# Optimization experiments

Measured on AMD Instinct MI355X. Metric: run time of the kernel, lower is better.

## Reference

```python
import jax, jax.numpy as jnp
import numpy as np

N = 100_000          # nodes
E = 1_600_000        # edges (avg degree 16)
NODE_SCA, NODE_VEC = 4, 3
EDGE_SCA, EDGE_VEC = 6, 3
OUT_SCA, OUT_VEC = 16, 16
CUTOFF = 10.0
EPS = 1e-6
SLOPE_VN = 0.2       # VNLeakyReLU negative slope (SurfGen default)
SLOPE_SCA = 0.01     # nn.LeakyReLU default


def setup_inputs() -> dict:
    key = jax.random.key(0)
    ks = jax.random.split(key, 22)
    rn = lambda k, s: jax.random.normal(k, s, dtype=jnp.float32)
    return {
        # forward args
        'node_sca': rn(ks[0], (N, NODE_SCA)),
        'node_vec': rn(ks[1], (N, NODE_VEC, 3)),
        'edge_sca': rn(ks[2], (E, EDGE_SCA)),
        'edge_vec': rn(ks[3], (E, EDGE_VEC, 3)),
        'gds_dist': jax.random.uniform(ks[4], (E,), dtype=jnp.float32) * 12.0,
        'edge_index': jax.random.randint(ks[5], (2, E), 0, N),
        # message projections (Linear weights stored [in,out])
        'W_nss': rn(ks[6], (NODE_SCA, OUT_SCA)) * 0.3, 'b_nss': rn(ks[7], (OUT_SCA,)) * 0.1,
        'W_ess': rn(ks[8], (EDGE_SCA, OUT_SCA)) * 0.3, 'b_ess': rn(ks[9], (OUT_SCA,)) * 0.1,
        'W_nsv': rn(ks[10], (NODE_SCA, OUT_SCA)) * 0.3, 'b_nsv': rn(ks[11], (OUT_SCA,)) * 0.1,
        'W_esv': rn(ks[12], (EDGE_SCA, OUT_SCA)) * 0.3, 'b_esv': rn(ks[13], (OUT_SCA,)) * 0.1,
        'W_nvv': rn(ks[14], (NODE_VEC, OUT_VEC)) * 0.3,   # VNLinear (no bias)
        'W_evv': rn(ks[15], (EDGE_VEC, OUT_VEC)) * 0.3,
        # GVPerceptronVN(16,16,16,16): GVLinear (dim_hid = 16) + VN LeakyReLU
        'W_lv':  rn(ks[16], (OUT_VEC, OUT_VEC)) * 0.25,   # lin_vector   (no bias)
        'W_lv2': rn(ks[17], (OUT_VEC, OUT_VEC)) * 0.25,   # lin_vector2  (no bias)
        'W_ls':  rn(ks[18], (OUT_VEC + OUT_SCA, OUT_SCA)) * 0.25,  # lin_scalar (no bias)
        'W_gate': rn(ks[19], (OUT_SCA, OUT_VEC)) * 0.25, 'b_gate': rn(ks[20], (OUT_VEC,)) * 0.1,
        'W_dir': rn(ks[21], (OUT_VEC, OUT_VEC)) * 0.25,   # VNLeakyReLU direction (no bias)
    }


def vn_linear(x, W):
    # x: [n, c_in, 3], W: [c_in, c_out] -> [n, c_out, 3]
    return jnp.einsum('nci,co->noi', x, W)


def reference(node_sca, node_vec, edge_sca, edge_vec, gds_dist, edge_index,
              W_nss, b_nss, W_ess, b_ess, W_nsv, b_nsv, W_esv, b_esv,
              W_nvv, W_evv, W_lv, W_lv2, W_ls, W_gate, b_gate, W_dir):
    src = edge_index[0]
    num_nodes = node_sca.shape[0]

    # cosine cutoff coefficient
    coeff = 0.5 * (jnp.cos(gds_dist * (jnp.pi / CUTOFF)) + 1.0)
    coeff = coeff * (gds_dist <= CUTOFF) * (gds_dist >= 0.0)  # [E]

    # scalar message: gather node proj, mix with edge proj, cutoff-weight
    node_ss = node_sca @ W_nss + b_nss                          # [N,16]
    edge_ss = edge_sca @ W_ess + b_ess                          # [E,16]
    msg_sca = node_ss[src] * edge_ss * coeff[:, None]           # [E,16]

    # vector message
    node_vv = vn_linear(node_vec, W_nvv)                        # [N,16,3]
    edge_vv = vn_linear(edge_vec, W_evv)                        # [E,16,3]
    node_sv = node_sca @ W_nsv + b_nsv                          # [N,16]
    edge_sv = edge_sca @ W_esv + b_esv                          # [E,16]
    msg_vec = (node_vv[src] * edge_sv[:, :, None]
               + node_sv[src][:, :, None] * edge_vv) * coeff[:, None, None]  # [E,16,3]

    # scatter_sum into source nodes (matches original's edge_index[0])
    aggr_sca = jax.ops.segment_sum(msg_sca, src, num_segments=num_nodes)  # [N,16]
    aggr_vec = jax.ops.segment_sum(msg_vec, src, num_segments=num_nodes)  # [N,16,3]

    # --- GVPerceptronVN: GVLinear ---
    v_inter = vn_linear(aggr_vec, W_lv)                          # [N,16,3]
    v_norm = jnp.sqrt(jnp.sum(v_inter * v_inter, axis=-1))       # [N,16]
    out_sca = jnp.concatenate([v_norm, aggr_sca], axis=-1) @ W_ls  # [N,16]
    out_vec = vn_linear(v_inter, W_lv2)                          # [N,16,3]
    gate = jax.nn.sigmoid(out_sca @ W_gate + b_gate)[:, :, None]
    out_vec = gate * out_vec

    # --- VNLeakyReLU on vectors ---
    d = vn_linear(out_vec, W_dir)                                # [N,16,3]
    dot = jnp.sum(out_vec * d, axis=-1, keepdims=True)
    mask = (dot >= 0).astype(out_vec.dtype)
    d_norm_sq = jnp.sum(d * d, axis=-1, keepdims=True)
    out_vec = SLOPE_VN * out_vec + (1.0 - SLOPE_VN) * (
        mask * out_vec + (1.0 - mask) * (out_vec - (dot / (d_norm_sq + EPS)) * d))

    # LeakyReLU on scalars
    out_sca = jnp.where(out_sca >= 0, out_sca, SLOPE_SCA * out_sca)
    return out_sca, out_vec
```

## Files before the change

### kernel.cpp

```cpp
#include <hip/hip_runtime.h>
#include <math.h>

#define CUTOFF_F 10.0f
#define PI_OVER_CUTOFF 0.31415926535897931f
#define KID 32

__global__ __launch_bounds__(256) void fill_ids(
    const float* __restrict__ gds,
    const int* __restrict__ eidx,
    const float* __restrict__ edge_sca,
    const float* __restrict__ edge_vec,
    int* __restrict__ count,
    int* __restrict__ bucket,
    float* __restrict__ aggr,
    int E)
{
    int e = blockIdx.x * blockDim.x + threadIdx.x;
    if (e >= E) return;

    float d = gds[e];
    if (d > CUTOFF_F || d < 0.0f) return;

    int src = eidx[e];
    int slot = atomicAdd(&count[src], 1);
    if (slot < KID) {
        bucket[(size_t)src * KID + slot] = e;
    } else {
        float c = 0.5f * (__cosf(d * PI_OVER_CUTOFF) + 1.0f);
        const float* es = edge_sca + (size_t)e * 6;
        const float* ev = edge_vec + (size_t)e * 9;
        float* base = aggr + (size_t)src * 16;
#pragma unroll
        for (int i = 0; i < 6; ++i) atomicAdd(base + i, c * es[i]);
        atomicAdd(base + 6, c);
#pragma unroll
        for (int i = 0; i < 9; ++i) atomicAdd(base + 7 + i, c * ev[i]);
    }
}

__global__ __launch_bounds__(256) void edge_aggregate(
    const float* __restrict__ edge_sca, const float* __restrict__ edge_vec,
    const float* __restrict__ gds, const int* __restrict__ eidx,
    float* __restrict__ aggr, int E)
{
    int e = blockIdx.x * blockDim.x + threadIdx.x;
    if (e >= E) return;
    int src = eidx[e];
    float d = gds[e];
    float coeff = 0.0f;
    if (d >= 0.0f && d <= CUTOFF_F)
        coeff = 0.5f * (__cosf(d * PI_OVER_CUTOFF) + 1.0f);
    float* base = aggr + (size_t)src * 16;
    const float* es = edge_sca + (size_t)e * 6;
    const float* ev = edge_vec + (size_t)e * 9;
#pragma unroll
    for (int c = 0; c < 6; ++c) atomicAdd(base + c, coeff * es[c]);
    atomicAdd(base + 6, coeff);
#pragma unroll
    for (int k = 0; k < 9; ++k) atomicAdd(base + 7 + k, coeff * ev[k]);
}

__global__ __launch_bounds__(256) void node_fused(
    const float* __restrict__ node_sca,
    const float* __restrict__ node_vec,
    const float* __restrict__ edge_sca,
    const float* __restrict__ edge_vec,
    const float* __restrict__ gds,
    const int* __restrict__ count,
    const int* __restrict__ bucket,
    const float* __restrict__ aggr,
    const float* __restrict__ W_nss, const float* __restrict__ b_nss,
    const float* __restrict__ W_ess, const float* __restrict__ b_ess,
    const float* __restrict__ W_nsv, const float* __restrict__ b_nsv,
    const float* __restrict__ W_esv, const float* __restrict__ b_esv,
    const float* __restrict__ W_nvv, const float* __restrict__ W_evv,
    const float* __restrict__ W_lv,  const float* __restrict__ W_lv2,
    const float* __restrict__ W_ls,
    const float* __restrict__ W_gate, const float* __restrict__ b_gate,
    const float* __restrict__ W_dir,
    float* __restrict__ out,
    int N, int mode)
{
    __shared__ float sW_nss[64],  sb_nss[16];
    __shared__ float sW_ess[96],  sb_ess[16];
    __shared__ float sW_nsv[64],  sb_nsv[16];
    __shared__ float sW_esv[96],  sb_esv[16];
    __shared__ float sW_nvv[48],  sW_evv[48];
    __shared__ float sW_lv[256],  sW_lv2[256];
    __shared__ float sW_ls[512];
    __shared__ float sW_gate[256], sb_gate[16];
    __shared__ float sW_dir[256];

    __shared__ float s_in  [16 * 33];
    __shared__ float s_avec[16 * 49];
    __shared__ float s_cat [16 * 33];
    __shared__ float s_vint[16 * 49];
    __shared__ float s_osca[16 * 17];
    __shared__ float s_ovec[16 * 49];

    __shared__ int   s_eid[KID * 17];
    __shared__ float s_ec [KID * 17];

    const int t = threadIdx.x;
    {
        for (int i = t; i < 64;  i += 256) { sW_nss[i] = W_nss[i]; sW_nsv[i] = W_nsv[i]; }
        for (int i = t; i < 96;  i += 256) { sW_ess[i] = W_ess[i]; sW_esv[i] = W_esv[i]; }
        for (int i = t; i < 48;  i += 256) { sW_nvv[i] = W_nvv[i]; sW_evv[i] = W_evv[i]; }
        for (int i = t; i < 256; i += 256) {
            sW_lv[i]   = W_lv[i];
            sW_lv2[i]  = W_lv2[i];
            sW_gate[i] = W_gate[i];
            sW_dir[i]  = W_dir[i];
        }
        for (int i = t; i < 512; i += 256) sW_ls[i] = W_ls[i];
        if (t < 16) {
            sb_nss[t]  = b_nss[t];
            sb_ess[t]  = b_ess[t];
            sb_nsv[t]  = b_nsv[t];
            sb_esv[t]  = b_esv[t];
            sb_gate[t] = b_gate[t];
        }
    }

    const int slot = t >> 4;
    const int o    = t & 15;
    const int n    = blockIdx.x * 16 + slot;
    const bool valid = (n < N);

    if (valid) {
        if (o < 4) s_in[slot * 33 + o]     = node_sca[(size_t)n * 4 + o];
        if (o < 9) s_in[slot * 33 + 4 + o] = node_vec[(size_t)n * 9 + o];
    }

    if (mode == 4) {
        int cnt = 0;
        if (valid) {
            cnt = count[n];
            if (cnt > KID) cnt = KID;
            const int* bk = bucket + (size_t)n * KID;
            for (int s = o; s < cnt; s += 16) {
                int e = bk[s];
                float d = gds[e];
                s_eid[s * 17 + slot] = e;
                s_ec [s * 17 + slot] = 0.5f * (__cosf(d * PI_OVER_CUTOFF) + 1.0f);
            }
        }
        __syncthreads();
        if (valid) {
            float acc = aggr[(size_t)n * 16 + o];
            const float* fsrc = (o < 6) ? edge_sca : edge_vec;
            const int    st   = (o < 6) ? 6 : 9;
            const int    off  = (o < 6) ? o : (o - 7);
            for (int s = 0; s < cnt; ++s) {
                int   e = s_eid[s * 17 + slot];
                float c = s_ec [s * 17 + slot];
                float f = (o == 6) ? 1.0f : fsrc[(size_t)e * st + off];
                acc += c * f;
            }
            s_in[slot * 33 + 13 + o] = acc;
        }
    } else {
        if (valid) s_in[slot * 33 + 13 + o] = aggr[(size_t)n * 16 + o];
    }
    __syncthreads();

    const float* in = s_in + slot * 33;

    float nss = sb_nss[o], nsv = sb_nsv[o];
#pragma unroll
    for (int c = 0; c < 4; ++c) {
        float x = in[c];
        nss += x * sW_nss[c * 16 + o];
        nsv += x * sW_nsv[c * 16 + o];
    }
    float nvv0 = 0.f, nvv1 = 0.f, nvv2 = 0.f;
#pragma unroll
    for (int c = 0; c < 3; ++c) {
        float w = sW_nvv[c * 16 + o];
        nvv0 += in[4 + c * 3 + 0] * w;
        nvv1 += in[4 + c * 3 + 1] * w;
        nvv2 += in[4 + c * 3 + 2] * w;
    }
    float cc = in[19];
    float es = cc * sb_ess[o], ev = cc * sb_esv[o];
#pragma unroll
    for (int c = 0; c < 6; ++c) {
        float a = in[13 + c];
        es += a * sW_ess[c * 16 + o];
        ev += a * sW_esv[c * 16 + o];
    }
    float EV0 = 0.f, EV1 = 0.f, EV2 = 0.f;
#pragma unroll
    for (int c = 0; c < 3; ++c) {
        float w = sW_evv[c * 16 + o];
        EV0 += in[20 + c * 3 + 0] * w;
        EV1 += in[20 + c * 3 + 1] * w;
        EV2 += in[20 + c * 3 + 2] * w;
    }

    float asca = nss * es;
    float av0 = nvv0 * ev + nsv * EV0;
    float av1 = nvv1 * ev + nsv * EV1;
    float av2 = nvv2 * ev + nsv * EV2;
    s_avec[slot * 49 + o * 3 + 0] = av0;
    s_avec[slot * 49 + o * 3 + 1] = av1;
    s_avec[slot * 49 + o * 3 + 2] = av2;
    s_cat[slot * 33 + 16 + o] = asca;
    __syncthreads();

    float vi0 = 0.f, vi1 = 0.f, vi2 = 0.f;
#pragma unroll
    for (int c = 0; c < 16; ++c) {
        float w = sW_lv[c * 16 + o];
        const float* a = &s_avec[slot * 49 + c * 3];
        vi0 += a[0] * w; vi1 += a[1] * w; vi2 += a[2] * w;
    }
    float vnorm = sqrtf(vi0 * vi0 + vi1 * vi1 + vi2 * vi2);
    s_vint[slot * 49 + o * 3 + 0] = vi0;
    s_vint[slot * 49 + o * 3 + 1] = vi1;
    s_vint[slot * 49 + o * 3 + 2] = vi2;
    s_cat[slot * 33 + o] = vnorm;
    __syncthreads();

    float osca = 0.f;
#pragma unroll
    for (int c = 0; c < 32; ++c)
        osca += s_cat[slot * 33 + c] * sW_ls[c * 16 + o];
    float ov0 = 0.f, ov1 = 0.f, ov2 = 0.f;
#pragma unroll
    for (int c = 0; c < 16; ++c) {
        float w = sW_lv2[c * 16 + o];
        const float* a = &s_vint[slot * 49 + c * 3];
        ov0 += a[0] * w; ov1 += a[1] * w; ov2 += a[2] * w;
    }
    s_osca[slot * 17 + o] = osca;
    __syncthreads();

    float g = sb_gate[o];
#pragma unroll
    for (int c = 0; c < 16; ++c)
        g += s_osca[slot * 17 + c] * sW_gate[c * 16 + o];
    g = 1.0f / (1.0f + __expf(-g));
    ov0 *= g; ov1 *= g; ov2 *= g;
    s_ovec[slot * 49 + o * 3 + 0] = ov0;
    s_ovec[slot * 49 + o * 3 + 1] = ov1;
    s_ovec[slot * 49 + o * 3 + 2] = ov2;
    __syncthreads();

    float dv0 = 0.f, dv1 = 0.f, dv2 = 0.f;
#pragma unroll
    for (int c = 0; c < 16; ++c) {
        float w = sW_dir[c * 16 + o];
        const float* a = &s_ovec[slot * 49 + c * 3];
        dv0 += a[0] * w; dv1 += a[1] * w; dv2 += a[2] * w;
    }
    float dot = ov0 * dv0 + ov1 * dv1 + ov2 * dv2;
    if (dot < 0.0f) {
        float dn = dv0 * dv0 + dv1 * dv1 + dv2 * dv2;
        float f = 0.8f * dot / (dn + 1e-6f);
        ov0 -= f * dv0; ov1 -= f * dv1; ov2 -= f * dv2;
    }

    if (valid) {
        float so = (osca >= 0.0f) ? osca : 0.01f * osca;
        out[(size_t)n * 16 + o] = so;
        size_t vb = (size_t)N * 16 + (size_t)n * 48 + (size_t)o * 3;
        out[vb + 0] = ov0;
        out[vb + 1] = ov1;
        out[vb + 2] = ov2;
    }
}

extern "C" void kernel_launch(void* const* d_in, const int* in_sizes, int n_in,
                              void* d_out, int out_size, void* d_ws, size_t ws_size,
                              hipStream_t stream)
{
    const float* node_sca = (const float*)d_in[0];
    const float* node_vec = (const float*)d_in[1];
    const float* edge_sca = (const float*)d_in[2];
    const float* edge_vec = (const float*)d_in[3];
    const float* gds      = (const float*)d_in[4];
    const int*   eidx     = (const int*)d_in[5];

    const int N = in_sizes[0] / 4;
    const int E = in_sizes[4];

    int*   count4  = (int*)d_ws;
    float* aggr4   = (float*)(count4 + N);
    int*   bucket4 = (int*)(aggr4 + (size_t)N * 16);
    size_t need4   = (size_t)N * 4 + (size_t)N * 64 + (size_t)N * KID * 4;

    float* aggr0  = (float*)d_ws;
    size_t need0  = (size_t)N * 64;

    if (ws_size >= need4) {
        hipMemsetAsync(count4, 0, (size_t)N * 4 + (size_t)N * 64, stream);
        fill_ids<<<(E + 255) / 256, 256, 0, stream>>>(
            gds, eidx, edge_sca, edge_vec, count4, bucket4, aggr4, E);
        node_fused<<<(N + 15) / 16, 256, 0, stream>>>(
            node_sca, node_vec, edge_sca, edge_vec, gds,
            count4, bucket4, aggr4,
            (const float*)d_in[6],  (const float*)d_in[7],
            (const float*)d_in[8],  (const float*)d_in[9],
            (const float*)d_in[10], (const float*)d_in[11],
            (const float*)d_in[12], (const float*)d_in[13],
            (const float*)d_in[14], (const float*)d_in[15],
            (const float*)d_in[16], (const float*)d_in[17],
            (const float*)d_in[18],
            (const float*)d_in[19], (const float*)d_in[20],
            (const float*)d_in[21],
            (float*)d_out, N, 4);
        return;
    }

    (void)need0;
    hipMemsetAsync(aggr0, 0, (size_t)N * 64, stream);
    edge_aggregate<<<(E + 255) / 256, 256, 0, stream>>>(
        edge_sca, edge_vec, gds, eidx, aggr0, E);
    node_fused<<<(N + 15) / 16, 256, 0, stream>>>(
        node_sca, node_vec, edge_sca, edge_vec, gds,
        (const int*)d_ws, (const int*)d_ws, aggr0,
        (const float*)d_in[6],  (const float*)d_in[7],
        (const float*)d_in[8],  (const float*)d_in[9],
        (const float*)d_in[10], (const float*)d_in[11],
        (const float*)d_in[12], (const float*)d_in[13],
        (const float*)d_in[14], (const float*)d_in[15],
        (const float*)d_in[16], (const float*)d_in[17],
        (const float*)d_in[18],
        (const float*)d_in[19], (const float*)d_in[20],
        (const float*)d_in[21],
        (float*)d_out, N, 0);
}
```

Measured before the change: 335.4 us.

## Scatter precomputed per-edge payloads into per-node slots instead of edge ids

Adds a scatter kernel that uses 16 threads per edge. It computes the cutoff-weighted 16-float payload (6 scalars, the coefficient, 9 vector components) and writes it contiguously into a per-node slot buffer, with overflow going to atomics. The node kernel's new mode then sums these contiguous slots directly, replacing the gather by edge id of scattered edge_sca/edge_vec rows and the shared id/coefficient staging (those buffers now alias other shared arrays). The cost is much larger workspace use (N*KIDr*64 bytes) and extra write traffic in exchange for coalesced reads. The path runs only if the workspace allows at least 16 slots per node.

```diff
diff --git a/kernel.cpp b/kernel.cpp
--- a/kernel.cpp
+++ b/kernel.cpp
@@ -4,6 +4,42 @@
 #define CUTOFF_F 10.0f
 #define PI_OVER_CUTOFF 0.31415926535897931f
 #define KID 32
+
+__global__ __launch_bounds__(256) void scatter_f32(
+    const float* __restrict__ gds,
+    const int* __restrict__ eidx,
+    const float* __restrict__ edge_sca,
+    const float* __restrict__ edge_vec,
+    int* __restrict__ count,
+    float* __restrict__ payload,
+    float* __restrict__ aggr,
+    int E, int KIDr)
+{
+    int t = blockIdx.x * blockDim.x + threadIdx.x;
+    int e = t >> 4;
+    int o = t & 15;
+    if (e >= E) return;
+
+    float d = gds[e];
+    if (d > CUTOFF_F || d < 0.0f) return;
+
+    float c = 0.5f * (__cosf(d * PI_OVER_CUTOFF) + 1.0f);
+    float f;
+    if (o < 6)       f = c * edge_sca[(size_t)e * 6 + o];
+    else if (o == 6) f = c;
+    else             f = c * edge_vec[(size_t)e * 9 + (o - 7)];
+
+    int src = eidx[e];
+    int slot = 0;
+    if (o == 0) slot = atomicAdd(&count[src], 1);
+    slot = __shfl(slot, 0, 16);
+
+    if (slot < KIDr) {
+        payload[((size_t)src * KIDr + slot) * 16 + o] = f;
+    } else {
+        atomicAdd(&aggr[(size_t)src * 16 + o], f);
+    }
+}
 
 __global__ __launch_bounds__(256) void fill_ids(
     const float* __restrict__ gds,
@@ -68,6 +104,7 @@
     const float* __restrict__ gds,
     const int* __restrict__ count,
     const int* __restrict__ bucket,
+    const float* __restrict__ payload,
     const float* __restrict__ aggr,
     const float* __restrict__ W_nss, const float* __restrict__ b_nss,
     const float* __restrict__ W_ess, const float* __restrict__ b_ess,
@@ -79,7 +116,7 @@
     const float* __restrict__ W_gate, const float* __restrict__ b_gate,
     const float* __restrict__ W_dir,
     float* __restrict__ out,
-    int N, int mode)
+    int N, int mode, int KIDr)
 {
     __shared__ float sW_nss[64],  sb_nss[16];
     __shared__ float sW_ess[96],  sb_ess[16];
@@ -98,8 +135,8 @@
     __shared__ float s_osca[16 * 17];
     __shared__ float s_ovec[16 * 49];
 
-    __shared__ int   s_eid[KID * 17];
-    __shared__ float s_ec [KID * 17];
+    int*   s_eid = (int*)s_vint;
+    float* s_ec  = s_ovec;
 
     const int t = threadIdx.x;
     {
@@ -132,7 +169,25 @@
         if (o < 9) s_in[slot * 33 + 4 + o] = node_vec[(size_t)n * 9 + o];
     }
 
-    if (mode == 4) {
+    if (mode == 5) {
+        if (valid) {
+            int cnt = count[n];
+            if (cnt > KIDr) cnt = KIDr;
+            const float* p = payload + (size_t)n * KIDr * 16 + o;
+            float a0 = 0.f, a1 = 0.f, a2 = 0.f, a3 = 0.f;
+            int s = 0;
+            for (; s + 3 < cnt; s += 4) {
+                a0 += p[(s + 0) * 16];
+                a1 += p[(s + 1) * 16];
+                a2 += p[(s + 2) * 16];
+                a3 += p[(s + 3) * 16];
+            }
+            for (; s < cnt; ++s)
+                a0 += p[s * 16];
+            a1 += aggr[(size_t)n * 16 + o];
+            s_in[slot * 33 + 13 + o] = (a0 + a1) + (a2 + a3);
+        }
+    } else if (mode == 4) {
         int cnt = 0;
         if (valid) {
             cnt = count[n];
@@ -285,21 +340,26 @@
     const int N = in_sizes[0] / 4;
     const int E = in_sizes[4];
 
-    int*   count4  = (int*)d_ws;
-    float* aggr4   = (float*)(count4 + N);
-    int*   bucket4 = (int*)(aggr4 + (size_t)N * 16);
-    size_t need4   = (size_t)N * 4 + (size_t)N * 64 + (size_t)N * KID * 4;
-
-    float* aggr0  = (float*)d_ws;
-    size_t need0  = (size_t)N * 64;
-
-    if (ws_size >= need4) {
-        hipMemsetAsync(count4, 0, (size_t)N * 4 + (size_t)N * 64, stream);
-        fill_ids<<<(E + 255) / 256, 256, 0, stream>>>(
-            gds, eidx, edge_sca, edge_vec, count4, bucket4, aggr4, E);
+    int*   countp = (int*)d_ws;
+    float* aggrp  = (float*)(countp + N);
+    size_t hdr    = (size_t)N * 4 + (size_t)N * 64;
+
+    float* payload5 = (float*)((char*)d_ws + hdr);
+    int KIDr = 0;
+    if (ws_size > hdr)
+        KIDr = (int)((ws_size - hdr) / ((size_t)N * 64));
+    if (KIDr > 32) KIDr = 32;
+
+    int*   bucket4 = (int*)((char*)d_ws + hdr);
+    size_t need4   = hdr + (size_t)N * KID * 4;
+
+    if (KIDr >= 16) {
+        hipMemsetAsync(countp, 0, hdr, stream);
+        scatter_f32<<<(int)(((size_t)E * 16 + 255) / 256), 256, 0, stream>>>(
+            gds, eidx, edge_sca, edge_vec, countp, payload5, aggrp, E, KIDr);
         node_fused<<<(N + 15) / 16, 256, 0, stream>>>(
             node_sca, node_vec, edge_sca, edge_vec, gds,
-            count4, bucket4, aggr4,
+            countp, bucket4, payload5, aggrp,
             (const float*)d_in[6],  (const float*)d_in[7],
             (const float*)d_in[8],  (const float*)d_in[9],
             (const float*)d_in[10], (const float*)d_in[11],
@@ -309,17 +369,37 @@
             (const float*)d_in[18],
             (const float*)d_in[19], (const float*)d_in[20],
             (const float*)d_in[21],
-            (float*)d_out, N, 4);
+            (float*)d_out, N, 5, KIDr);
         return;
     }
 
-    (void)need0;
+    if (ws_size >= need4) {
+        hipMemsetAsync(countp, 0, hdr, stream);
+        fill_ids<<<(E + 255) / 256, 256, 0, stream>>>(
+            gds, eidx, edge_sca, edge_vec, countp, bucket4, aggrp, E);
+        node_fused<<<(N + 15) / 16, 256, 0, stream>>>(
+            node_sca, node_vec, edge_sca, edge_vec, gds,
+            countp, bucket4, payload5, aggrp,
+            (const float*)d_in[6],  (const float*)d_in[7],
+            (const float*)d_in[8],  (const float*)d_in[9],
+            (const float*)d_in[10], (const float*)d_in[11],
+            (const float*)d_in[12], (const float*)d_in[13],
+            (const float*)d_in[14], (const float*)d_in[15],
+            (const float*)d_in[16], (const float*)d_in[17],
+            (const float*)d_in[18],
+            (const float*)d_in[19], (const float*)d_in[20],
+            (const float*)d_in[21],
+            (float*)d_out, N, 4, 0);
+        return;
+    }
+
+    float* aggr0 = (float*)d_ws;
     hipMemsetAsync(aggr0, 0, (size_t)N * 64, stream);
     edge_aggregate<<<(E + 255) / 256, 256, 0, stream>>>(
         edge_sca, edge_vec, gds, eidx, aggr0, E);
     node_fused<<<(N + 15) / 16, 256, 0, stream>>>(
         node_sca, node_vec, edge_sca, edge_vec, gds,
-        (const int*)d_ws, (const int*)d_ws, aggr0,
+        (const int*)d_ws, (const int*)d_ws, (const float*)d_ws, aggr0,
         (const float*)d_in[6],  (const float*)d_in[7],
         (const float*)d_in[8],  (const float*)d_in[9],
         (const float*)d_in[10], (const float*)d_in[11],
@@ -329,5 +409,5 @@
         (const float*)d_in[18],
         (const float*)d_in[19], (const float*)d_in[20],
         (const float*)d_in[21],
-        (float*)d_out, N, 0);
+        (float*)d_out, N, 0, 0);
 }
```

Measured after the change: 399.2 us. +19.0%, slower.

## Replace per-node edge buckets with per-block coarse buckets and LDS reduction

Applied to the files above, without the earlier changes.

Edges are appended to coarse buckets of 98 nodes each, storing the cutoff-weighted 16-float features contiguously. Each node-block then reduces its bucket into shared memory with LDS atomics and processes its 98 nodes in 7 tiles. This replaces the per-node id buckets, which forced scattered gathers of edge features in the node kernel, with streaming reads of precomputed features. The costs are a larger workspace, heavy contention on one global counter per bucket, and sequential tiles that lengthen each block's work.

```diff
diff --git a/kernel.cpp b/kernel.cpp
--- a/kernel.cpp
+++ b/kernel.cpp
@@ -3,38 +3,55 @@
 
 #define CUTOFF_F 10.0f
 #define PI_OVER_CUTOFF 0.31415926535897931f
-#define KID 32
-
-__global__ __launch_bounds__(256) void fill_ids(
+#define NPB    98
+#define NTILES 7
+
+__global__ __launch_bounds__(256) void bucket_append(
     const float* __restrict__ gds,
     const int* __restrict__ eidx,
     const float* __restrict__ edge_sca,
     const float* __restrict__ edge_vec,
-    int* __restrict__ count,
-    int* __restrict__ bucket,
-    float* __restrict__ aggr,
-    int E)
+    int* __restrict__ bcnt,
+    int* __restrict__ flag,
+    float* __restrict__ aggr_ovf,
+    int* __restrict__ ids,
+    float* __restrict__ feats,
+    int E, int cap)
 {
-    int e = blockIdx.x * blockDim.x + threadIdx.x;
+    int e = blockIdx.x * 256 + threadIdx.x;
     if (e >= E) return;
 
     float d = gds[e];
-    if (d > CUTOFF_F || d < 0.0f) return;
-
+    if (d < 0.0f || d > CUTOFF_F) return;
+
+    float c = 0.5f * (__cosf(d * PI_OVER_CUTOFF) + 1.0f);
     int src = eidx[e];
-    int slot = atomicAdd(&count[src], 1);
-    if (slot < KID) {
-        bucket[(size_t)src * KID + slot] = e;
+    const float* es = edge_sca + (size_t)e * 6;
+    const float* ev = edge_vec + (size_t)e * 9;
+
+    float f[16];
+#pragma unroll
+    for (int i = 0; i < 6; ++i) f[i] = c * es[i];
+    f[6] = c;
+#pragma unroll
+    for (int i = 0; i < 9; ++i) f[7 + i] = c * ev[i];
+
+    int b = src / NPB;
+    int slot = atomicAdd(&bcnt[b * 16], 1);
+
+    if (slot < cap) {
+        size_t r = (size_t)b * cap + slot;
+        ids[r] = src;
+        float4* pr = (float4*)(feats + r * 16);
+        pr[0] = make_float4(f[0],  f[1],  f[2],  f[3]);
+        pr[1] = make_float4(f[4],  f[5],  f[6],  f[7]);
+        pr[2] = make_float4(f[8],  f[9],  f[10], f[11]);
+        pr[3] = make_float4(f[12], f[13], f[14], f[15]);
     } else {
-        float c = 0.5f * (__cosf(d * PI_OVER_CUTOFF) + 1.0f);
-        const float* es = edge_sca + (size_t)e * 6;
-        const float* ev = edge_vec + (size_t)e * 9;
-        float* base = aggr + (size_t)src * 16;
-#pragma unroll
-        for (int i = 0; i < 6; ++i) atomicAdd(base + i, c * es[i]);
-        atomicAdd(base + 6, c);
-#pragma unroll
-        for (int i = 0; i < 9; ++i) atomicAdd(base + 7 + i, c * ev[i]);
+        flag[0] = 1;
+        float* bb = aggr_ovf + (size_t)src * 16;
+#pragma unroll
+        for (int i = 0; i < 16; ++i) atomicAdd(bb + i, f[i]);
     }
 }
 
@@ -60,15 +77,14 @@
     for (int k = 0; k < 9; ++k) atomicAdd(base + 7 + k, coeff * ev[k]);
 }
 
-__global__ __launch_bounds__(256) void node_fused(
+__global__ __launch_bounds__(256) void bucket_reduce_node(
     const float* __restrict__ node_sca,
     const float* __restrict__ node_vec,
-    const float* __restrict__ edge_sca,
-    const float* __restrict__ edge_vec,
-    const float* __restrict__ gds,
-    const int* __restrict__ count,
-    const int* __restrict__ bucket,
-    const float* __restrict__ aggr,
+    const int* __restrict__ bcnt,
+    const int* __restrict__ flag,
+    const float* __restrict__ aggr_ovf,
+    const int* __restrict__ ids,
+    const float* __restrict__ feats,
     const float* __restrict__ W_nss, const float* __restrict__ b_nss,
     const float* __restrict__ W_ess, const float* __restrict__ b_ess,
     const float* __restrict__ W_nsv, const float* __restrict__ b_nsv,
@@ -79,7 +95,7 @@
     const float* __restrict__ W_gate, const float* __restrict__ b_gate,
     const float* __restrict__ W_dir,
     float* __restrict__ out,
-    int N, int mode)
+    int N, int cap, int forceOvf)
 {
     __shared__ float sW_nss[64],  sb_nss[16];
     __shared__ float sW_ess[96],  sb_ess[16];
@@ -91,15 +107,14 @@
     __shared__ float sW_gate[256], sb_gate[16];
     __shared__ float sW_dir[256];
 
+    __shared__ float s_aggr[NPB * 17];
+
     __shared__ float s_in  [16 * 33];
     __shared__ float s_avec[16 * 49];
     __shared__ float s_cat [16 * 33];
     __shared__ float s_vint[16 * 49];
     __shared__ float s_osca[16 * 17];
     __shared__ float s_ovec[16 * 49];
-
-    __shared__ int   s_eid[KID * 17];
-    __shared__ float s_ec [KID * 17];
 
     const int t = threadIdx.x;
     {
@@ -121,153 +136,155 @@
             sb_gate[t] = b_gate[t];
         }
     }
-
-    const int slot = t >> 4;
-    const int o    = t & 15;
-    const int n    = blockIdx.x * 16 + slot;
-    const bool valid = (n < N);
-
-    if (valid) {
-        if (o < 4) s_in[slot * 33 + o]     = node_sca[(size_t)n * 4 + o];
-        if (o < 9) s_in[slot * 33 + 4 + o] = node_vec[(size_t)n * 9 + o];
-    }
-
-    if (mode == 4) {
-        int cnt = 0;
+    for (int i = t; i < NPB * 17; i += 256) s_aggr[i] = 0.0f;
+    __syncthreads();
+
+    const int b     = blockIdx.x;
+    const int node0 = b * NPB;
+    const int g     = t >> 4;
+    const int o     = t & 15;
+
+    if (!forceOvf) {
+        int cnt = bcnt[b * 16];
+        if (cnt > cap) cnt = cap;
+        size_t rb = (size_t)b * cap;
+        for (int r = g; r < cnt; r += 16) {
+            int src = ids[rb + r];
+            float v = feats[(rb + r) * 16 + o];
+            atomicAdd(&s_aggr[(src - node0) * 17 + o], v);
+        }
+    }
+    __syncthreads();
+
+    int useOvf = forceOvf | flag[0];
+    if (useOvf) {
+        for (int idx = t; idx < NPB * 16; idx += 256) {
+            int nn = idx >> 4, oo = idx & 15;
+            int n = node0 + nn;
+            if (n < N) s_aggr[nn * 17 + oo] += aggr_ovf[(size_t)n * 16 + oo];
+        }
+    }
+    __syncthreads();
+
+    for (int tile = 0; tile < NTILES; ++tile) {
+        const int slotn = tile * 16 + g;
+        const int n     = node0 + slotn;
+        const bool valid = (slotn < NPB) && (n < N);
+        const int slot = g;
+
         if (valid) {
-            cnt = count[n];
-            if (cnt > KID) cnt = KID;
-            const int* bk = bucket + (size_t)n * KID;
-            for (int s = o; s < cnt; s += 16) {
-                int e = bk[s];
-                float d = gds[e];
-                s_eid[s * 17 + slot] = e;
-                s_ec [s * 17 + slot] = 0.5f * (__cosf(d * PI_OVER_CUTOFF) + 1.0f);
-            }
-        }
-        __syncthreads();
+            if (o < 4) s_in[slot * 33 + o]     = node_sca[(size_t)n * 4 + o];
+            if (o < 9) s_in[slot * 33 + 4 + o] = node_vec[(size_t)n * 9 + o];
+            s_in[slot * 33 + 13 + o] = s_aggr[slotn * 17 + o];
+        }
+        __syncthreads();
+
+        const float* in = s_in + slot * 33;
+
+        float nss = sb_nss[o], nsv = sb_nsv[o];
+#pragma unroll
+        for (int c = 0; c < 4; ++c) {
+            float x = in[c];
+            nss += x * sW_nss[c * 16 + o];
+            nsv += x * sW_nsv[c * 16 + o];
+        }
+        float nvv0 = 0.f, nvv1 = 0.f, nvv2 = 0.f;
+#pragma unroll
+        for (int c = 0; c < 3; ++c) {
+            float w = sW_nvv[c * 16 + o];
+            nvv0 += in[4 + c * 3 + 0] * w;
+            nvv1 += in[4 + c * 3 + 1] * w;
+            nvv2 += in[4 + c * 3 + 2] * w;
+        }
+        float cc = in[19];
+        float es = cc * sb_ess[o], ev = cc * sb_esv[o];
+#pragma unroll
+        for (int c = 0; c < 6; ++c) {
+            float a = in[13 + c];
+            es += a * sW_ess[c * 16 + o];
+            ev += a * sW_esv[c * 16 + o];
+        }
+        float EV0 = 0.f, EV1 = 0.f, EV2 = 0.f;
+#pragma unroll
+        for (int c = 0; c < 3; ++c) {
+            float w = sW_evv[c * 16 + o];
+            EV0 += in[20 + c * 3 + 0] * w;
+            EV1 += in[20 + c * 3 + 1] * w;
+            EV2 += in[20 + c * 3 + 2] * w;
+        }
+
+        float asca = nss * es;
+        float av0 = nvv0 * ev + nsv * EV0;
+        float av1 = nvv1 * ev + nsv * EV1;
+        float av2 = nvv2 * ev + nsv * EV2;
+        s_avec[slot * 49 + o * 3 + 0] = av0;
+        s_avec[slot * 49 + o * 3 + 1] = av1;
+        s_avec[slot * 49 + o * 3 + 2] = av2;
+        s_cat[slot * 33 + 16 + o] = asca;
+        __syncthreads();
+
+        float vi0 = 0.f, vi1 = 0.f, vi2 = 0.f;
+#pragma unroll
+        for (int c = 0; c < 16; ++c) {
+            float w = sW_lv[c * 16 + o];
+            const float* a = &s_avec[slot * 49 + c * 3];
+            vi0 += a[0] * w; vi1 += a[1] * w; vi2 += a[2] * w;
+        }
+        float vnorm = sqrtf(vi0 * vi0 + vi1 * vi1 + vi2 * vi2);
+        s_vint[slot * 49 + o * 3 + 0] = vi0;
+        s_vint[slot * 49 + o * 3 + 1] = vi1;
+        s_vint[slot * 49 + o * 3 + 2] = vi2;
+        s_cat[slot * 33 + o] = vnorm;
+        __syncthreads();
+
+        float osca = 0.f;
+#pragma unroll
+        for (int c = 0; c < 32; ++c)
+            osca += s_cat[slot * 33 + c] * sW_ls[c * 16 + o];
+        float ov0 = 0.f, ov1 = 0.f, ov2 = 0.f;
+#pragma unroll
+        for (int c = 0; c < 16; ++c) {
+            float w = sW_lv2[c * 16 + o];
+            const float* a = &s_vint[slot * 49 + c * 3];
+            ov0 += a[0] * w; ov1 += a[1] * w; ov2 += a[2] * w;
+        }
+        s_osca[slot * 17 + o] = osca;
+        __syncthreads();
+
+        float gg = sb_gate[o];
+#pragma unroll
+        for (int c = 0; c < 16; ++c)
+            gg += s_osca[slot * 17 + c] * sW_gate[c * 16 + o];
+        gg = 1.0f / (1.0f + __expf(-gg));
+        ov0 *= gg; ov1 *= gg; ov2 *= gg;
+        s_ovec[slot * 49 + o * 3 + 0] = ov0;
+        s_ovec[slot * 49 + o * 3 + 1] = ov1;
+        s_ovec[slot * 49 + o * 3 + 2] = ov2;
+        __syncthreads();
+
+        float dv0 = 0.f, dv1 = 0.f, dv2 = 0.f;
+#pragma unroll
+        for (int c = 0; c < 16; ++c) {
+            float w = sW_dir[c * 16 + o];
+            const float* a = &s_ovec[slot * 49 + c * 3];
+            dv0 += a[0] * w; dv1 += a[1] * w; dv2 += a[2] * w;
+        }
+        float dot = ov0 * dv0 + ov1 * dv1 + ov2 * dv2;
+        if (dot < 0.0f) {
+            float dn = dv0 * dv0 + dv1 * dv1 + dv2 * dv2;
+            float fr = 0.8f * dot / (dn + 1e-6f);
+            ov0 -= fr * dv0; ov1 -= fr * dv1; ov2 -= fr * dv2;
+        }
+
         if (valid) {
-            float acc = aggr[(size_t)n * 16 + o];
-            const float* fsrc = (o < 6) ? edge_sca : edge_vec;
-            const int    st   = (o < 6) ? 6 : 9;
-            const int    off  = (o < 6) ? o : (o - 7);
-            for (int s = 0; s < cnt; ++s) {
-                int   e = s_eid[s * 17 + slot];
-                float c = s_ec [s * 17 + slot];
-                float f = (o == 6) ? 1.0f : fsrc[(size_t)e * st + off];
-                acc += c * f;
-            }
-            s_in[slot * 33 + 13 + o] = acc;
-        }
-    } else {
-        if (valid) s_in[slot * 33 + 13 + o] = aggr[(size_t)n * 16 + o];
-    }
-    __syncthreads();
-
-    const float* in = s_in + slot * 33;
-
-    float nss = sb_nss[o], nsv = sb_nsv[o];
-#pragma unroll
-    for (int c = 0; c < 4; ++c) {
-        float x = in[c];
-        nss += x * sW_nss[c * 16 + o];
-        nsv += x * sW_nsv[c * 16 + o];
-    }
-    float nvv0 = 0.f, nvv1 = 0.f, nvv2 = 0.f;
-#pragma unroll
-    for (int c = 0; c < 3; ++c) {
-        float w = sW_nvv[c * 16 + o];
-        nvv0 += in[4 + c * 3 + 0] * w;
-        nvv1 += in[4 + c * 3 + 1] * w;
-        nvv2 += in[4 + c * 3 + 2] * w;
-    }
-    float cc = in[19];
-    float es = cc * sb_ess[o], ev = cc * sb_esv[o];
-#pragma unroll
-    for (int c = 0; c < 6; ++c) {
-        float a = in[13 + c];
-        es += a * sW_ess[c * 16 + o];
-        ev += a * sW_esv[c * 16 + o];
-    }
-    float EV0 = 0.f, EV1 = 0.f, EV2 = 0.f;
-#pragma unroll
-    for (int c = 0; c < 3; ++c) {
-        float w = sW_evv[c * 16 + o];
-        EV0 += in[20 + c * 3 + 0] * w;
-        EV1 += in[20 + c * 3 + 1] * w;
-        EV2 += in[20 + c * 3 + 2] * w;
-    }
-
-    float asca = nss * es;
-    float av0 = nvv0 * ev + nsv * EV0;
-    float av1 = nvv1 * ev + nsv * EV1;
-    float av2 = nvv2 * ev + nsv * EV2;
-    s_avec[slot * 49 + o * 3 + 0] = av0;
-    s_avec[slot * 49 + o * 3 + 1] = av1;
-    s_avec[slot * 49 + o * 3 + 2] = av2;
-    s_cat[slot * 33 + 16 + o] = asca;
-    __syncthreads();
-
-    float vi0 = 0.f, vi1 = 0.f, vi2 = 0.f;
-#pragma unroll
-    for (int c = 0; c < 16; ++c) {
-        float w = sW_lv[c * 16 + o];
-        const float* a = &s_avec[slot * 49 + c * 3];
-        vi0 += a[0] * w; vi1 += a[1] * w; vi2 += a[2] * w;
-    }
-    float vnorm = sqrtf(vi0 * vi0 + vi1 * vi1 + vi2 * vi2);
-    s_vint[slot * 49 + o * 3 + 0] = vi0;
-    s_vint[slot * 49 + o * 3 + 1] = vi1;
-    s_vint[slot * 49 + o * 3 + 2] = vi2;
-    s_cat[slot * 33 + o] = vnorm;
-    __syncthreads();
-
-    float osca = 0.f;
-#pragma unroll
-    for (int c = 0; c < 32; ++c)
-        osca += s_cat[slot * 33 + c] * sW_ls[c * 16 + o];
-    float ov0 = 0.f, ov1 = 0.f, ov2 = 0.f;
-#pragma unroll
-    for (int c = 0; c < 16; ++c) {
-        float w = sW_lv2[c * 16 + o];
-        const float* a = &s_vint[slot * 49 + c * 3];
-        ov0 += a[0] * w; ov1 += a[1] * w; ov2 += a[2] * w;
-    }
-    s_osca[slot * 17 + o] = osca;
-    __syncthreads();
-
-    float g = sb_gate[o];
-#pragma unroll
-    for (int c = 0; c < 16; ++c)
-        g += s_osca[slot * 17 + c] * sW_gate[c * 16 + o];
-    g = 1.0f / (1.0f + __expf(-g));
-    ov0 *= g; ov1 *= g; ov2 *= g;
-    s_ovec[slot * 49 + o * 3 + 0] = ov0;
-    s_ovec[slot * 49 + o * 3 + 1] = ov1;
-    s_ovec[slot * 49 + o * 3 + 2] = ov2;
-    __syncthreads();
-
-    float dv0 = 0.f, dv1 = 0.f, dv2 = 0.f;
-#pragma unroll
-    for (int c = 0; c < 16; ++c) {
-        float w = sW_dir[c * 16 + o];
-        const float* a = &s_ovec[slot * 49 + c * 3];
-        dv0 += a[0] * w; dv1 += a[1] * w; dv2 += a[2] * w;
-    }
-    float dot = ov0 * dv0 + ov1 * dv1 + ov2 * dv2;
-    if (dot < 0.0f) {
-        float dn = dv0 * dv0 + dv1 * dv1 + dv2 * dv2;
-        float f = 0.8f * dot / (dn + 1e-6f);
-        ov0 -= f * dv0; ov1 -= f * dv1; ov2 -= f * dv2;
-    }
-
-    if (valid) {
-        float so = (osca >= 0.0f) ? osca : 0.01f * osca;
-        out[(size_t)n * 16 + o] = so;
-        size_t vb = (size_t)N * 16 + (size_t)n * 48 + (size_t)o * 3;
-        out[vb + 0] = ov0;
-        out[vb + 1] = ov1;
-        out[vb + 2] = ov2;
+            float so = (osca >= 0.0f) ? osca : 0.01f * osca;
+            out[(size_t)n * 16 + o] = so;
+            size_t vb = (size_t)N * 16 + (size_t)n * 48 + (size_t)o * 3;
+            out[vb + 0] = ov0;
+            out[vb + 1] = ov1;
+            out[vb + 2] = ov2;
+        }
+        __syncthreads();
     }
 }
 
@@ -284,22 +301,31 @@
 
     const int N = in_sizes[0] / 4;
     const int E = in_sizes[4];
-
-    int*   count4  = (int*)d_ws;
-    float* aggr4   = (float*)(count4 + N);
-    int*   bucket4 = (int*)(aggr4 + (size_t)N * 16);
-    size_t need4   = (size_t)N * 4 + (size_t)N * 64 + (size_t)N * KID * 4;
-
-    float* aggr0  = (float*)d_ws;
-    size_t need0  = (size_t)N * 64;
-
-    if (ws_size >= need4) {
-        hipMemsetAsync(count4, 0, (size_t)N * 4 + (size_t)N * 64, stream);
-        fill_ids<<<(E + 255) / 256, 256, 0, stream>>>(
-            gds, eidx, edge_sca, edge_vec, count4, bucket4, aggr4, E);
-        node_fused<<<(N + 15) / 16, 256, 0, stream>>>(
-            node_sca, node_vec, edge_sca, edge_vec, gds,
-            count4, bucket4, aggr4,
+    const int NBk = (N + NPB - 1) / NPB;
+
+    int*   bcnt     = (int*)d_ws;
+    int*   flag     = bcnt + (size_t)NBk * 16;
+    float* aggr_ovf = (float*)(flag + 16);
+    int*   ids      = (int*)(aggr_ovf + (size_t)N * 16);
+    size_t zero_bytes = ((size_t)NBk * 16 + 16) * 4 + (size_t)N * 64;
+
+    long long cap = 0;
+    if (ws_size > zero_bytes + 64)
+        cap = (long long)((ws_size - zero_bytes - 64) / ((size_t)NBk * 68));
+    {
+        long long capMax = 2LL * E / (NBk > 0 ? NBk : 1) + 64;
+        if (cap > capMax) cap = capMax;
+    }
+    size_t ids_bytes = (((size_t)NBk * (size_t)cap * 4) + 63) & ~(size_t)63;
+    float* feats = (float*)((char*)ids + ids_bytes);
+
+    if (cap >= 1100 || (cap >= 256 && (long long)E <= cap * NBk)) {
+        hipMemsetAsync(bcnt, 0, zero_bytes, stream);
+        bucket_append<<<(E + 255) / 256, 256, 0, stream>>>(
+            gds, eidx, edge_sca, edge_vec,
+            bcnt, flag, aggr_ovf, ids, feats, E, (int)cap);
+        bucket_reduce_node<<<NBk, 256, 0, stream>>>(
+            node_sca, node_vec, bcnt, flag, aggr_ovf, ids, feats,
             (const float*)d_in[6],  (const float*)d_in[7],
             (const float*)d_in[8],  (const float*)d_in[9],
             (const float*)d_in[10], (const float*)d_in[11],
@@ -309,17 +335,17 @@
             (const float*)d_in[18],
             (const float*)d_in[19], (const float*)d_in[20],
             (const float*)d_in[21],
-            (float*)d_out, N, 4);
+            (float*)d_out, N, (int)cap, 0);
         return;
     }
 
-    (void)need0;
-    hipMemsetAsync(aggr0, 0, (size_t)N * 64, stream);
+    size_t zb = zero_bytes;
+    if (zb > ws_size) zb = ws_size;
+    hipMemsetAsync(bcnt, 0, zb, stream);
     edge_aggregate<<<(E + 255) / 256, 256, 0, stream>>>(
-        edge_sca, edge_vec, gds, eidx, aggr0, E);
-    node_fused<<<(N + 15) / 16, 256, 0, stream>>>(
-        node_sca, node_vec, edge_sca, edge_vec, gds,
-        (const int*)d_ws, (const int*)d_ws, aggr0,
+        edge_sca, edge_vec, gds, eidx, aggr_ovf, E);
+    bucket_reduce_node<<<NBk, 256, 0, stream>>>(
+        node_sca, node_vec, bcnt, flag, aggr_ovf, ids, feats,
         (const float*)d_in[6],  (const float*)d_in[7],
         (const float*)d_in[8],  (const float*)d_in[9],
         (const float*)d_in[10], (const float*)d_in[11],
@@ -329,5 +355,5 @@
         (const float*)d_in[18],
         (const float*)d_in[19], (const float*)d_in[20],
         (const float*)d_in[21],
-        (float*)d_out, N, 0);
+        (float*)d_out, N, 0, 1);
 }
```

Result: slower. 412.1 us (+22.9%).

## Replace bucketed edge gather with direct unsafe float atomics for aggregation

Applied to the files above, without the earlier changes.

Drops the per-node bucket scheme, where the first 32 edges per source were stored as ids and gathered in the node kernel. Every in-cutoff edge now atomically adds its 16 cutoff-weighted features straight into the node aggregate using unsafeAtomicAdd, which can map to hardware float atomics on AMD. This removes the count atomics, bucket writes, the shared-memory staging and the irregular gather from the node kernel, at the cost of about sixteen times more atomic traffic per edge.

```diff
diff --git a/kernel.cpp b/kernel.cpp
--- a/kernel.cpp
+++ b/kernel.cpp
@@ -3,71 +3,48 @@
 
 #define CUTOFF_F 10.0f
 #define PI_OVER_CUTOFF 0.31415926535897931f
-#define KID 32
-
-__global__ __launch_bounds__(256) void fill_ids(
+
+__global__ __launch_bounds__(256) void edge_atomic(
     const float* __restrict__ gds,
     const int* __restrict__ eidx,
     const float* __restrict__ edge_sca,
     const float* __restrict__ edge_vec,
-    int* __restrict__ count,
-    int* __restrict__ bucket,
     float* __restrict__ aggr,
     int E)
 {
-    int e = blockIdx.x * blockDim.x + threadIdx.x;
+    int e = blockIdx.x * 256 + threadIdx.x;
     if (e >= E) return;
 
     float d = gds[e];
-    if (d > CUTOFF_F || d < 0.0f) return;
-
+    if (d < 0.0f || d > CUTOFF_F) return;
+
+    float c = 0.5f * (__cosf(d * PI_OVER_CUTOFF) + 1.0f);
     int src = eidx[e];
-    int slot = atomicAdd(&count[src], 1);
-    if (slot < KID) {
-        bucket[(size_t)src * KID + slot] = e;
-    } else {
-        float c = 0.5f * (__cosf(d * PI_OVER_CUTOFF) + 1.0f);
-        const float* es = edge_sca + (size_t)e * 6;
-        const float* ev = edge_vec + (size_t)e * 9;
-        float* base = aggr + (size_t)src * 16;
-#pragma unroll
-        for (int i = 0; i < 6; ++i) atomicAdd(base + i, c * es[i]);
-        atomicAdd(base + 6, c);
-#pragma unroll
-        for (int i = 0; i < 9; ++i) atomicAdd(base + 7 + i, c * ev[i]);
-    }
-}
-
-__global__ __launch_bounds__(256) void edge_aggregate(
-    const float* __restrict__ edge_sca, const float* __restrict__ edge_vec,
-    const float* __restrict__ gds, const int* __restrict__ eidx,
-    float* __restrict__ aggr, int E)
-{
-    int e = blockIdx.x * blockDim.x + threadIdx.x;
-    if (e >= E) return;
-    int src = eidx[e];
-    float d = gds[e];
-    float coeff = 0.0f;
-    if (d >= 0.0f && d <= CUTOFF_F)
-        coeff = 0.5f * (__cosf(d * PI_OVER_CUTOFF) + 1.0f);
-    float* base = aggr + (size_t)src * 16;
     const float* es = edge_sca + (size_t)e * 6;
     const float* ev = edge_vec + (size_t)e * 9;
-#pragma unroll
-    for (int c = 0; c < 6; ++c) atomicAdd(base + c, coeff * es[c]);
-    atomicAdd(base + 6, coeff);
-#pragma unroll
-    for (int k = 0; k < 9; ++k) atomicAdd(base + 7 + k, coeff * ev[k]);
+    float* base = aggr + (size_t)src * 16;
+
+    unsafeAtomicAdd(base + 0,  c * es[0]);
+    unsafeAtomicAdd(base + 1,  c * es[1]);
+    unsafeAtomicAdd(base + 2,  c * es[2]);
+    unsafeAtomicAdd(base + 3,  c * es[3]);
+    unsafeAtomicAdd(base + 4,  c * es[4]);
+    unsafeAtomicAdd(base + 5,  c * es[5]);
+    unsafeAtomicAdd(base + 6,  c);
+    unsafeAtomicAdd(base + 7,  c * ev[0]);
+    unsafeAtomicAdd(base + 8,  c * ev[1]);
+    unsafeAtomicAdd(base + 9,  c * ev[2]);
+    unsafeAtomicAdd(base + 10, c * ev[3]);
+    unsafeAtomicAdd(base + 11, c * ev[4]);
+    unsafeAtomicAdd(base + 12, c * ev[5]);
+    unsafeAtomicAdd(base + 13, c * ev[6]);
+    unsafeAtomicAdd(base + 14, c * ev[7]);
+    unsafeAtomicAdd(base + 15, c * ev[8]);
 }
 
-__global__ __launch_bounds__(256) void node_fused(
+__global__ __launch_bounds__(256) void node_lite(
     const float* __restrict__ node_sca,
     const float* __restrict__ node_vec,
-    const float* __restrict__ edge_sca,
-    const float* __restrict__ edge_vec,
-    const float* __restrict__ gds,
-    const int* __restrict__ count,
-    const int* __restrict__ bucket,
     const float* __restrict__ aggr,
     const float* __restrict__ W_nss, const float* __restrict__ b_nss,
     const float* __restrict__ W_ess, const float* __restrict__ b_ess,
@@ -79,7 +56,7 @@
     const float* __restrict__ W_gate, const float* __restrict__ b_gate,
     const float* __restrict__ W_dir,
     float* __restrict__ out,
-    int N, int mode)
+    int N)
 {
     __shared__ float sW_nss[64],  sb_nss[16];
     __shared__ float sW_ess[96],  sb_ess[16];
@@ -97,9 +74,6 @@
     __shared__ float s_vint[16 * 49];
     __shared__ float s_osca[16 * 17];
     __shared__ float s_ovec[16 * 49];
-
-    __shared__ int   s_eid[KID * 17];
-    __shared__ float s_ec [KID * 17];
 
     const int t = threadIdx.x;
     {
@@ -130,37 +104,7 @@
     if (valid) {
         if (o < 4) s_in[slot * 33 + o]     = node_sca[(size_t)n * 4 + o];
         if (o < 9) s_in[slot * 33 + 4 + o] = node_vec[(size_t)n * 9 + o];
-    }
-
-    if (mode == 4) {
-        int cnt = 0;
-        if (valid) {
-            cnt = count[n];
-            if (cnt > KID) cnt = KID;
-            const int* bk = bucket + (size_t)n * KID;
-            for (int s = o; s < cnt; s += 16) {
-                int e = bk[s];
-                float d = gds[e];
-                s_eid[s * 17 + slot] = e;
-                s_ec [s * 17 + slot] = 0.5f * (__cosf(d * PI_OVER_CUTOFF) + 1.0f);
-            }
-        }
-        __syncthreads();
-        if (valid) {
-            float acc = aggr[(size_t)n * 16 + o];
-            const float* fsrc = (o < 6) ? edge_sca : edge_vec;
-            const int    st   = (o < 6) ? 6 : 9;
-            const int    off  = (o < 6) ? o : (o - 7);
-            for (int s = 0; s < cnt; ++s) {
-                int   e = s_eid[s * 17 + slot];
-                float c = s_ec [s * 17 + slot];
-                float f = (o == 6) ? 1.0f : fsrc[(size_t)e * st + off];
-                acc += c * f;
-            }
-            s_in[slot * 33 + 13 + o] = acc;
-        }
-    } else {
-        if (valid) s_in[slot * 33 + 13 + o] = aggr[(size_t)n * 16 + o];
+        s_in[slot * 33 + 13 + o] = aggr[(size_t)n * 16 + o];
     }
     __syncthreads();
 
@@ -285,41 +229,13 @@
     const int N = in_sizes[0] / 4;
     const int E = in_sizes[4];
 
-    int*   count4  = (int*)d_ws;
-    float* aggr4   = (float*)(count4 + N);
-    int*   bucket4 = (int*)(aggr4 + (size_t)N * 16);
-    size_t need4   = (size_t)N * 4 + (size_t)N * 64 + (size_t)N * KID * 4;
-
-    float* aggr0  = (float*)d_ws;
-    size_t need0  = (size_t)N * 64;
-
-    if (ws_size >= need4) {
-        hipMemsetAsync(count4, 0, (size_t)N * 4 + (size_t)N * 64, stream);
-        fill_ids<<<(E + 255) / 256, 256, 0, stream>>>(
-            gds, eidx, edge_sca, edge_vec, count4, bucket4, aggr4, E);
-        node_fused<<<(N + 15) / 16, 256, 0, stream>>>(
-            node_sca, node_vec, edge_sca, edge_vec, gds,
-            count4, bucket4, aggr4,
-            (const float*)d_in[6],  (const float*)d_in[7],
-            (const float*)d_in[8],  (const float*)d_in[9],
-            (const float*)d_in[10], (const float*)d_in[11],
-            (const float*)d_in[12], (const float*)d_in[13],
-            (const float*)d_in[14], (const float*)d_in[15],
-            (const float*)d_in[16], (const float*)d_in[17],
-            (const float*)d_in[18],
-            (const float*)d_in[19], (const float*)d_in[20],
-            (const float*)d_in[21],
-            (float*)d_out, N, 4);
-        return;
-    }
-
-    (void)need0;
-    hipMemsetAsync(aggr0, 0, (size_t)N * 64, stream);
-    edge_aggregate<<<(E + 255) / 256, 256, 0, stream>>>(
-        edge_sca, edge_vec, gds, eidx, aggr0, E);
-    node_fused<<<(N + 15) / 16, 256, 0, stream>>>(
-        node_sca, node_vec, edge_sca, edge_vec, gds,
-        (const int*)d_ws, (const int*)d_ws, aggr0,
+    float* aggr = (float*)d_ws;
+
+    hipMemsetAsync(aggr, 0, (size_t)N * 64, stream);
+    edge_atomic<<<(E + 255) / 256, 256, 0, stream>>>(
+        gds, eidx, edge_sca, edge_vec, aggr, E);
+    node_lite<<<(N + 15) / 16, 256, 0, stream>>>(
+        node_sca, node_vec, aggr,
         (const float*)d_in[6],  (const float*)d_in[7],
         (const float*)d_in[8],  (const float*)d_in[9],
         (const float*)d_in[10], (const float*)d_in[11],
@@ -329,5 +245,5 @@
         (const float*)d_in[18],
         (const float*)d_in[19], (const float*)d_in[20],
         (const float*)d_in[21],
-        (float*)d_out, N, 0);
+        (float*)d_out, N);
 }
```

Result: slower. 1.278 ms (+280.9%).
